# Performance work log

Measured on AMD Instinct MI355X. Metric: run time of the kernel, lower is better.

## Reference

```python
import jax, jax.numpy as jnp
import numpy as np

N = 100000   # num_nodes
E = 300000   # num directed edges (symmetrized to 2E inside forward)
D = 128      # input_dim
O = 128      # output_dim
R = 32       # num_relations
B = 8        # num_bases


def setup_inputs() -> dict:
    key = jax.random.key(0)
    ks = jax.random.split(key, 8)
    x = jax.random.normal(ks[0], (N, D), dtype=jnp.float32)
    node_keep_mask = jax.random.randint(ks[1], (N,), 0, 2) > 0
    source = jax.random.randint(ks[2], (E,), 0, N, dtype=jnp.int32)
    target = jax.random.randint(ks[3], (E,), 0, N, dtype=jnp.int32)
    edge_type = jax.random.randint(ks[4], (E,), 0, R, dtype=jnp.int32)
    edge_weights = jax.random.uniform(ks[5], (E,), dtype=jnp.float32)
    # xavier_normal for bases
    std = (2.0 / (D + O)) ** 0.5
    bases = jax.random.normal(ks[6], (B, D, O), dtype=jnp.float32) * std
    # uniform then L1-normalized rows, shape (R+1, B); row R is the self-loop
    rbw = jax.random.uniform(ks[7], (R + 1, B), dtype=jnp.float32)
    rbw = rbw / jnp.sum(rbw, axis=1, keepdims=True)
    return {
        "x": x,
        "node_keep_mask": node_keep_mask,
        "source": source,
        "target": target,
        "edge_type": edge_type,
        "edge_weights": edge_weights,
        "bases": bases,
        "relation_base_weights": rbw,
    }


def reference(x, node_keep_mask, source, target, edge_type, edge_weights,
              bases, relation_base_weights):
    # Self-loop: weight for relation id == num_relations (last row)
    w_self = jnp.einsum("bij,b->ij", bases, relation_base_weights[-1])
    out = jnp.where(node_keep_mask[:, None], x @ w_self, jnp.zeros((), x.dtype))

    # Symmetrize edges: messages flow in both directions (same relation/weight)
    src = jnp.concatenate([source, target])          # (2E,)
    tgt = jnp.concatenate([target, source])          # (2E,)
    etype = jnp.concatenate([edge_type, edge_type])  # (2E,)
    ew = jnp.concatenate([edge_weights, edge_weights])  # (2E,)

    # Project all nodes through every basis once: (N, B, O)
    proj = jnp.einsum("nd,bdo->nbo", x, bases)
    # Per-edge basis coefficients from the edge's relation: (2E, B)
    coeff = relation_base_weights[etype]
    # Message: x[src] @ (sum_b coeff_b * base_b) == sum_b coeff_b * proj[src, b]
    msg = jnp.einsum("eb,ebo->eo", coeff, proj[src])  # (2E, O)
    msg = msg * ew[:, None]

    # Scatter-add messages into target nodes
    out = out.at[tgt].add(msg)
    return out
```

## Files before the change

kernel.cpp:

```cpp
#include <hip/hip_runtime.h>

typedef __attribute__((ext_vector_type(8))) __bf16 bf16x8;
typedef __attribute__((ext_vector_type(4))) float f32x4;
typedef __attribute__((ext_vector_type(8))) unsigned short ushortx8;

#define MC 384
#define MCP 448

__device__ inline unsigned short f2bf(float f) {
  unsigned int u = __float_as_uint(f);
  unsigned int r = (u + 0x7FFFu + ((u >> 16) & 1u)) >> 16;
  return (unsigned short)r;
}
__device__ inline float bflo(unsigned u) { return __uint_as_float(u << 16); }
__device__ inline float bfhi(unsigned u) { return __uint_as_float(u & 0xFFFF0000u); }

__global__ __launch_bounds__(256) void prep_kernel(const float* __restrict__ x,
                                                   unsigned short* __restrict__ xb, int total8,
                                                   const float* __restrict__ bases,
                                                   unsigned short* __restrict__ bmt,
                                                   const int* __restrict__ src,
                                                   const int* __restrict__ tgt, int E,
                                                   int* __restrict__ cnt,
                                                   const unsigned char* __restrict__ mask,
                                                   int mbytes, int* __restrict__ flag_out,
                                                   int CB, int TB, int HB) {
  int bid = blockIdx.x;
  if (bid < CB) {
    int id = bid * 256 + threadIdx.x;
    if (id >= total8) return;
    f32x4 f0 = ((const f32x4*)x)[2 * id];
    f32x4 f1 = ((const f32x4*)x)[2 * id + 1];
    ushortx8 r;
    r[0] = f2bf(f0[0]); r[1] = f2bf(f0[1]); r[2] = f2bf(f0[2]); r[3] = f2bf(f0[3]);
    r[4] = f2bf(f1[0]); r[5] = f2bf(f1[1]); r[6] = f2bf(f1[2]); r[7] = f2bf(f1[3]);
    ((ushortx8*)xb)[id] = r;
  } else if (bid < CB + TB) {
    int id = (bid - CB) * 256 + threadIdx.x;
    if (id >= 128 * 1024) return;
    int o = id >> 10, k = id & 1023, b = k >> 7, d = k & 127;
    bmt[id] = f2bf(bases[b * 16384 + d * 128 + o]);
  } else if (bid < CB + TB + HB) {
    int i = (bid - CB - TB) * 256 + threadIdx.x;
    if (i >= E) return;
    atomicAdd(&cnt[tgt[i]], 1);
    atomicAdd(&cnt[src[i]], 1);
  } else {
    __shared__ int nz_off, big;
    if (threadIdx.x == 0) { nz_off = 0; big = 0; }
    __syncthreads();
    int lnz = 0, lbig = 0;
    for (int i = threadIdx.x; i < mbytes; i += 256) {
      unsigned char v = mask[i];
      if ((i & 3) && v) lnz++;
      if (v > 1) lbig++;
    }
    if (lnz) atomicAdd(&nz_off, lnz);
    if (lbig) atomicAdd(&big, lbig);
    __syncthreads();
    if (threadIdx.x == 0) *flag_out = (nz_off == 0) ? 0 : ((big == 0) ? 1 : 2);
  }
}

__global__ __launch_bounds__(256) void scanA_kernel(const int* __restrict__ cnt, int N,
                                                    int* __restrict__ bsum) {
  __shared__ int s[256];
  int t = threadIdx.x, i = blockIdx.x * 256 + t;
  s[t] = (i < N) ? cnt[i] : 0;
  __syncthreads();
#pragma unroll
  for (int off = 128; off > 0; off >>= 1) {
    if (t < off) s[t] += s[t + off];
    __syncthreads();
  }
  if (t == 0) bsum[blockIdx.x] = s[0];
}

__global__ __launch_bounds__(256) void scanB_kernel(const int* __restrict__ cnt, int N,
                                                    const int* __restrict__ bsum, int NB,
                                                    int* __restrict__ base,
                                                    int* __restrict__ cursor) {
  __shared__ int s[256];
  __shared__ int spref;
  int t = threadIdx.x, bid = blockIdx.x;
  int acc = 0;
  for (int i = t; i < bid; i += 256) acc += bsum[i];
  s[t] = acc;
  __syncthreads();
#pragma unroll
  for (int off = 128; off > 0; off >>= 1) {
    if (t < off) s[t] += s[t + off];
    __syncthreads();
  }
  if (t == 0) spref = s[0];
  __syncthreads();
  int pref = spref;
  __syncthreads();
  int i = bid * 256 + t;
  int c = (i < N) ? cnt[i] : 0;
  s[t] = c;
  __syncthreads();
  for (int off = 1; off < 256; off <<= 1) {
    int x = (t >= off) ? s[t - off] : 0;
    __syncthreads();
    s[t] += x;
    __syncthreads();
  }
  if (i < N) {
    int v = pref + s[t] - c;
    base[i] = v;
    cursor[i] = v;
  }
  if (bid == NB - 1 && t == 255) base[N] = pref + s[255];
}

__global__ __launch_bounds__(256) void scatter_kernel(const int* __restrict__ src,
                                                      const int* __restrict__ tgt,
                                                      const int* __restrict__ et,
                                                      const float* __restrict__ ew, int E,
                                                      const float* __restrict__ rbw,
                                                      int* __restrict__ cursor,
                                                      unsigned* __restrict__ msrc,
                                                      uint4* __restrict__ mcoef) {
  __shared__ float ctab[264];
  for (int i = threadIdx.x; i < 264; i += 256) ctab[i] = rbw[i];
  __syncthreads();
  if (blockIdx.x == 0 && threadIdx.x < 80) {
    msrc[2 * E + threadIdx.x] = 0u;
    mcoef[2 * E + threadIdx.x] = make_uint4(0u, 0u, 0u, 0u);
  }
  int i = blockIdx.x * 256 + threadIdx.x;
  if (i >= E) return;
  int s = src[i], g = tgt[i], r = et[i];
  float w = ew[i];
  uint4 cv;
  {
    const float* c = &ctab[r * 8];
    cv.x = (unsigned)f2bf(w * c[0]) | ((unsigned)f2bf(w * c[1]) << 16);
    cv.y = (unsigned)f2bf(w * c[2]) | ((unsigned)f2bf(w * c[3]) << 16);
    cv.z = (unsigned)f2bf(w * c[4]) | ((unsigned)f2bf(w * c[5]) << 16);
    cv.w = (unsigned)f2bf(w * c[6]) | ((unsigned)f2bf(w * c[7]) << 16);
  }
  int s1 = atomicAdd(&cursor[g], 1);
  msrc[s1] = (unsigned)s;
  mcoef[s1] = cv;
  int s2 = atomicAdd(&cursor[s], 1);
  msrc[s2] = (unsigned)g;
  mcoef[s2] = cv;
}

template <bool LDSM>
__device__ __forceinline__ void load4(const uint2* __restrict__ xb64,
                                      const unsigned* lms, const unsigned* __restrict__ gms,
                                      int B0, int gcap, int locS, int mb, int ll,
                                      unsigned Nm1, uint2 (&xq)[4]) {
#pragma unroll
  for (int s = 0; s < 4; ++s) {
    int idx = locS + mb + s;
    unsigned row;
    if (LDSM) row = lms[min(idx, MCP - 1)];
    else      row = gms[min(B0 + idx, gcap)];
    row = min(row & 0xFFFFFu, Nm1);
    xq[s] = xb64[(size_t)row * 32 + ll];
  }
}

template <bool LDSM>
__device__ __forceinline__ void fma4(const uint4* lmc, const uint4* __restrict__ gmc,
                                     int B0, int gcap, int locS, int cntS, int mb,
                                     const uint2 (&xq)[4], f32x4 (&z)[8]) {
#pragma unroll
  for (int s = 0; s < 4; ++s) {
    int idx = locS + mb + s;
    uint4 cf;
    if (LDSM) cf = lmc[min(idx, MCP - 1)];
    else      cf = gmc[min(B0 + idx, gcap)];
    unsigned vm = ((mb + s) < cntS) ? 0xFFFFFFFFu : 0u;
    unsigned c0 = cf.x & vm, c1 = cf.y & vm, c2 = cf.z & vm, c3 = cf.w & vm;
    f32x4 xv = {bflo(xq[s].x), bfhi(xq[s].x), bflo(xq[s].y), bfhi(xq[s].y)};
    float a;
    a = bflo(c0); z[0] = __builtin_elementwise_fma((f32x4){a, a, a, a}, xv, z[0]);
    a = bfhi(c0); z[1] = __builtin_elementwise_fma((f32x4){a, a, a, a}, xv, z[1]);
    a = bflo(c1); z[2] = __builtin_elementwise_fma((f32x4){a, a, a, a}, xv, z[2]);
    a = bfhi(c1); z[3] = __builtin_elementwise_fma((f32x4){a, a, a, a}, xv, z[3]);
    a = bflo(c2); z[4] = __builtin_elementwise_fma((f32x4){a, a, a, a}, xv, z[4]);
    a = bfhi(c2); z[5] = __builtin_elementwise_fma((f32x4){a, a, a, a}, xv, z[5]);
    a = bflo(c3); z[6] = __builtin_elementwise_fma((f32x4){a, a, a, a}, xv, z[6]);
    a = bfhi(c3); z[7] = __builtin_elementwise_fma((f32x4){a, a, a, a}, xv, z[7]);
  }
}

template <bool LDSM>
__device__ __forceinline__ void duo_loop(const uint2* __restrict__ xb64,
                                         const unsigned* lms, const uint4* lmc,
                                         const unsigned* __restrict__ gms,
                                         const uint4* __restrict__ gmc,
                                         int B0, int gcap, int locS, int cntS, int rmax,
                                         int ll, unsigned Nm1, f32x4 (&z)[8]) {
  int rounds = (rmax + 3) >> 2;
  if (rounds <= 0) return;
  uint2 xq0[4], xq1[4];
  load4<LDSM>(xb64, lms, gms, B0, gcap, locS, 0, ll, Nm1, xq0);
  for (int r = 0; r < rounds; ++r) {
    if ((r & 1) == 0) {
      if (r + 1 < rounds) load4<LDSM>(xb64, lms, gms, B0, gcap, locS, (r + 1) * 4, ll, Nm1, xq1);
      fma4<LDSM>(lmc, gmc, B0, gcap, locS, cntS, r * 4, xq0, z);
    } else {
      if (r + 1 < rounds) load4<LDSM>(xb64, lms, gms, B0, gcap, locS, (r + 1) * 4, ll, Nm1, xq0);
      fma4<LDSM>(lmc, gmc, B0, gcap, locS, cntS, r * 4, xq1, z);
    }
  }
}

__global__ __launch_bounds__(512, 4) void gather_kernel(
    const uint2* __restrict__ xb64, const unsigned short* __restrict__ bmt,
    const int* __restrict__ base, const unsigned* __restrict__ msrc,
    const uint4* __restrict__ mcoef, const float* __restrict__ rbw,
    const void* __restrict__ maskp, const int* __restrict__ flag_p,
    float* __restrict__ out, int N, int gcap) {
  extern __shared__ char smem[];
  unsigned* lms = (unsigned*)(smem + 65536);
  uint4* lmc = (uint4*)(smem + 65536 + MCP * 4);
  int* lbase = (int*)(smem + 65536 + MCP * 4 + MCP * 16);
  int t = threadIdx.x;
  int wid = t >> 6, l = t & 63;
  int hw = l >> 5, ll = l & 31;
  int t0 = blockIdx.x * 32;
  int flag = *flag_p;
  unsigned Nm1 = (unsigned)(N - 1);

  if (t < 33) lbase[t] = base[min(t0 + t, N)];
  int B0 = __builtin_amdgcn_readfirstlane(base[min(t0, N)]);
  int B1 = __builtin_amdgcn_readfirstlane(base[min(t0 + 32, N)]);
  int nm = B1 - B0;
  bool use_lds = (nm <= MC);
  if (use_lds) {
    for (int i = t; i < nm; i += 512) {
      lms[i] = msrc[B0 + i];
      lmc[i] = mcoef[B0 + i];
    }
    int pz = nm + t;
    if (t < 64 && pz < MCP) {
      lms[pz] = 0u;
      lmc[pz] = make_uint4(0u, 0u, 0u, 0u);
    }
  }
  __syncthreads();

  for (int p = 0; p < 2; ++p) {
    int jA = wid * 4 + p * 2, jB = jA + 1;
    int tgA = t0 + jA, tgB = t0 + jB;
    int begA = __builtin_amdgcn_readfirstlane(lbase[jA]);
    int begB = __builtin_amdgcn_readfirstlane(lbase[jB]);
    int endB = __builtin_amdgcn_readfirstlane(lbase[jB + 1]);
    int cntA = (tgA < N) ? (begB - begA) : 0;
    int cntB = (tgB < N) ? (endB - begB) : 0;
    int locA = begA - B0, locB = begB - B0;
    int tgS = hw ? tgB : tgA;
    int tcS = min(tgS, N - 1);
    int locS = hw ? locB : locA;
    int cntS = hw ? cntB : cntA;
    uint2 xs = xb64[(size_t)tcS * 32 + ll];
    int keep;
    if (flag == 0)      keep = ((const int*)maskp)[tcS] != 0;
    else if (flag == 1) keep = ((const unsigned char*)maskp)[tcS] != 0;
    else                keep = ((const float*)maskp)[tcS] != 0.f;
    float ms = (keep && tgS < N) ? 1.f : 0.f;
    f32x4 xv0 = {bflo(xs.x), bfhi(xs.x), bflo(xs.y), bfhi(xs.y)};
    f32x4 z[8];
#pragma unroll
    for (int b = 0; b < 8; ++b) {
      float a = ms * rbw[256 + b];
      z[b] = (f32x4){a, a, a, a} * xv0;
    }
    int rmax = max(cntA, cntB);
    if (use_lds)
      duo_loop<true>(xb64, lms, lmc, msrc, mcoef, B0, gcap, locS, cntS, rmax, ll, Nm1, z);
    else
      duo_loop<false>(xb64, lms, lmc, msrc, mcoef, B0, gcap, locS, cntS, rmax, ll, Nm1, z);
    int rowS = hw ? jB : jA;
#pragma unroll
    for (int b = 0; b < 8; ++b) {
      unsigned d0 = (unsigned)f2bf(z[b][0]) | ((unsigned)f2bf(z[b][1]) << 16);
      unsigned d1 = (unsigned)f2bf(z[b][2]) | ((unsigned)f2bf(z[b][3]) << 16);
      int byte = rowS * 2048 + ((b * 256 + ll * 8) ^ ((rowS & 7) << 4));
      *(uint2*)(smem + byte) = make_uint2(d0, d1);
    }
  }
  __syncthreads();

  int l15 = l & 15, lk8 = (l >> 4) * 8;
  f32x4 acc[2] = {};
  for (int ks = 0; ks < 32; ++ks) {
    int k0 = ks * 32 + lk8;
    bf16x8 a[2], bb;
#pragma unroll
    for (int rt = 0; rt < 2; ++rt) {
      int tr = rt * 16 + l15;
      int byte = tr * 2048 + ((k0 * 2) ^ ((tr & 7) << 4));
      a[rt] = *(const bf16x8*)(smem + byte);
    }
    int col = wid * 16 + l15;
    bb = *(const bf16x8*)(bmt + (size_t)col * 1024 + k0);
#pragma unroll
    for (int rt = 0; rt < 2; ++rt)
      acc[rt] = __builtin_amdgcn_mfma_f32_16x16x32_bf16(a[rt], bb, acc[rt], 0, 0, 0);
  }
#pragma unroll
  for (int rt = 0; rt < 2; ++rt) {
    int rowb = t0 + rt * 16 + (l >> 4) * 4;
    int col = wid * 16 + l15;
#pragma unroll
    for (int i = 0; i < 4; ++i) {
      int row = rowb + i;
      if (row < N) out[(size_t)row * 128 + col] = acc[rt][i];
    }
  }
}

extern "C" void kernel_launch(void* const* d_in, const int* in_sizes, int n_in,
                              void* d_out, int out_size, void* d_ws, size_t ws_size,
                              hipStream_t stream) {
  const float* x = (const float*)d_in[0];
  const void* mask = d_in[1];
  const int* source = (const int*)d_in[2];
  const int* target = (const int*)d_in[3];
  const int* etype = (const int*)d_in[4];
  const float* eweight = (const float*)d_in[5];
  const float* bases = (const float*)d_in[6];
  const float* rbw = (const float*)d_in[7];
  float* out = (float*)d_out;

  const int N = in_sizes[1];
  const int E = in_sizes[2];
  const int M = 2 * E;
  const int NB = (N + 255) / 256;

  char* ws = (char*)d_ws;
  size_t off = 0;
  unsigned short* xb = (unsigned short*)(ws + off); off += (size_t)N * 256;
  unsigned short* bmt = (unsigned short*)(ws + off); off += 128 * 1024 * 2;
  unsigned* msrc = (unsigned*)(ws + off); off += (size_t)(M + 96) * 4;
  uint4* mcoef = (uint4*)(ws + off); off += (size_t)(M + 96) * 16;
  int* base = (int*)(ws + off); off += ((size_t)N + 64) * 4;
  int* cursor = (int*)(ws + off); off += ((size_t)N + 64) * 4;
  int* cnt = (int*)(ws + off); off += ((size_t)N + 64) * 4;
  int* bsum = (int*)(ws + off); off += 2048;
  int* flag = (int*)(ws + off); off += 256;

  hipMemsetAsync(cnt, 0, (size_t)N * 4, stream);
  int total8 = (N * 128) / 8;
  int CB = (total8 + 255) / 256;
  int TB = (128 * 1024 + 255) / 256;
  int HB = (E + 255) / 256;
  prep_kernel<<<CB + TB + HB + 1, 256, 0, stream>>>(x, xb, total8, bases, bmt,
                                                    source, target, E, cnt,
                                                    (const unsigned char*)mask,
                                                    N < 8192 ? N : 8192, flag, CB, TB, HB);
  scanA_kernel<<<NB, 256, 0, stream>>>(cnt, N, bsum);
  scanB_kernel<<<NB, 256, 0, stream>>>(cnt, N, bsum, NB, base, cursor);
  scatter_kernel<<<(E + 255) / 256, 256, 0, stream>>>(source, target, etype, eweight, E,
                                                      rbw, cursor, msrc, mcoef);
  int gblk = (N + 31) / 32;
  size_t shmem = 65536 + MCP * 4 + MCP * 16 + 136;
  gather_kernel<<<gblk, 512, shmem, stream>>>((const uint2*)xb, bmt, base, msrc, mcoef,
                                              rbw, mask, flag, out, N, M + 79);
}
```

Before: 236.6 us.

## Fuse two node-pair gather passes into one triple-buffered prefetch pipeline

The gather phase used to run two separate passes per wave, each with its own double-buffered prefetch loop. It now runs a single continuous loop over the rounds of both node pairs, with a three-deep prefetch ring, and flushes and reseeds the accumulators at the boundary between pairs. This keeps row loads in flight across the pair boundary and hides more latency, at the cost of more registers and per-round select logic. Separately, the bases transpose in the prep kernel now goes through a 32x33 shared-memory tile so that both reads and writes are coalesced.

```diff
diff --git a/kernel.cpp b/kernel.cpp
--- a/kernel.cpp
+++ b/kernel.cpp
@@ -25,6 +25,8 @@
                                                    const unsigned char* __restrict__ mask,
                                                    int mbytes, int* __restrict__ flag_out,
                                                    int CB, int TB, int HB) {
+  __shared__ float tile_s[32][33];
+  __shared__ int nz_off, big;
   int bid = blockIdx.x;
   if (bid < CB) {
     int id = bid * 256 + threadIdx.x;
@@ -36,17 +38,27 @@
     r[4] = f2bf(f1[0]); r[5] = f2bf(f1[1]); r[6] = f2bf(f1[2]); r[7] = f2bf(f1[3]);
     ((ushortx8*)xb)[id] = r;
   } else if (bid < CB + TB) {
-    int id = (bid - CB) * 256 + threadIdx.x;
-    if (id >= 128 * 1024) return;
-    int o = id >> 10, k = id & 1023, b = k >> 7, d = k & 127;
-    bmt[id] = f2bf(bases[b * 16384 + d * 128 + o]);
+    int bid2 = bid - CB;
+    int b = bid2 >> 4, tile = bid2 & 15;
+    int o0 = (tile >> 2) * 32, d0 = (tile & 3) * 32;
+    int tx = threadIdx.x & 31, ty = threadIdx.x >> 5;
+#pragma unroll
+    for (int i = 0; i < 4; ++i) {
+      int dl = ty + i * 8;
+      tile_s[dl][tx] = bases[b * 16384 + (d0 + dl) * 128 + (o0 + tx)];
+    }
+    __syncthreads();
+#pragma unroll
+    for (int i = 0; i < 4; ++i) {
+      int ol = ty + i * 8;
+      bmt[(size_t)(o0 + ol) * 1024 + b * 128 + d0 + tx] = f2bf(tile_s[tx][ol]);
+    }
   } else if (bid < CB + TB + HB) {
     int i = (bid - CB - TB) * 256 + threadIdx.x;
     if (i >= E) return;
     atomicAdd(&cnt[tgt[i]], 1);
     atomicAdd(&cnt[src[i]], 1);
   } else {
-    __shared__ int nz_off, big;
     if (threadIdx.x == 0) { nz_off = 0; big = 0; }
     __syncthreads();
     int lnz = 0, lbig = 0;
@@ -150,13 +162,17 @@
 }
 
 template <bool LDSM>
-__device__ __forceinline__ void load4(const uint2* __restrict__ xb64,
-                                      const unsigned* lms, const unsigned* __restrict__ gms,
-                                      int B0, int gcap, int locS, int mb, int ll,
-                                      unsigned Nm1, uint2 (&xq)[4]) {
+__device__ __forceinline__ void pf_round(const uint2* __restrict__ xb64,
+                                         const unsigned* lms, const unsigned* __restrict__ gms,
+                                         int B0, int gcap, int R0, int RT,
+                                         int loc0, int loc1, int q, int ll, unsigned Nm1,
+                                         uint2 (&xq)[4]) {
+  int qq = min(q, RT - 1);
+  int loc = (qq < R0) ? loc0 : loc1;
+  int m = ((qq < R0) ? qq : qq - R0) * 4;
 #pragma unroll
   for (int s = 0; s < 4; ++s) {
-    int idx = locS + mb + s;
+    int idx = loc + m + s;
     unsigned row;
     if (LDSM) row = lms[min(idx, MCP - 1)];
     else      row = gms[min(B0 + idx, gcap)];
@@ -166,16 +182,20 @@
 }
 
 template <bool LDSM>
-__device__ __forceinline__ void fma4(const uint4* lmc, const uint4* __restrict__ gmc,
-                                     int B0, int gcap, int locS, int cntS, int mb,
-                                     const uint2 (&xq)[4], f32x4 (&z)[8]) {
+__device__ __forceinline__ void fma_round(const uint4* lmc, const uint4* __restrict__ gmc,
+                                          int B0, int gcap, int R0,
+                                          int loc0, int cnt0, int loc1, int cnt1,
+                                          int r, const uint2 (&xq)[4], f32x4 (&z)[8]) {
+  int loc = (r < R0) ? loc0 : loc1;
+  int cnt = (r < R0) ? cnt0 : cnt1;
+  int mb = ((r < R0) ? r : r - R0) * 4;
 #pragma unroll
   for (int s = 0; s < 4; ++s) {
-    int idx = locS + mb + s;
+    int idx = loc + mb + s;
     uint4 cf;
     if (LDSM) cf = lmc[min(idx, MCP - 1)];
     else      cf = gmc[min(B0 + idx, gcap)];
-    unsigned vm = ((mb + s) < cntS) ? 0xFFFFFFFFu : 0u;
+    unsigned vm = ((mb + s) < cnt) ? 0xFFFFFFFFu : 0u;
     unsigned c0 = cf.x & vm, c1 = cf.y & vm, c2 = cf.z & vm, c3 = cf.w & vm;
     f32x4 xv = {bflo(xq[s].x), bfhi(xq[s].x), bflo(xq[s].y), bfhi(xq[s].y)};
     float a;
@@ -190,26 +210,59 @@
   }
 }
 
+__device__ __forceinline__ void seed_z(const float* __restrict__ rbw, float ms, uint2 xs,
+                                       f32x4 (&z)[8]) {
+  f32x4 xv0 = {bflo(xs.x), bfhi(xs.x), bflo(xs.y), bfhi(xs.y)};
+#pragma unroll
+  for (int b = 0; b < 8; ++b) {
+    float a = ms * rbw[256 + b];
+    z[b] = (f32x4){a, a, a, a} * xv0;
+  }
+}
+
+__device__ __forceinline__ void flush_z(char* smem, int rowS, int ll, const f32x4 (&z)[8]) {
+#pragma unroll
+  for (int b = 0; b < 8; ++b) {
+    unsigned d0 = (unsigned)f2bf(z[b][0]) | ((unsigned)f2bf(z[b][1]) << 16);
+    unsigned d1 = (unsigned)f2bf(z[b][2]) | ((unsigned)f2bf(z[b][3]) << 16);
+    int byte = rowS * 2048 + ((b * 256 + ll * 8) ^ ((rowS & 7) << 4));
+    *(uint2*)(smem + byte) = make_uint2(d0, d1);
+  }
+}
+
 template <bool LDSM>
-__device__ __forceinline__ void duo_loop(const uint2* __restrict__ xb64,
-                                         const unsigned* lms, const uint4* lmc,
-                                         const unsigned* __restrict__ gms,
-                                         const uint4* __restrict__ gmc,
-                                         int B0, int gcap, int locS, int cntS, int rmax,
-                                         int ll, unsigned Nm1, f32x4 (&z)[8]) {
-  int rounds = (rmax + 3) >> 2;
-  if (rounds <= 0) return;
-  uint2 xq0[4], xq1[4];
-  load4<LDSM>(xb64, lms, gms, B0, gcap, locS, 0, ll, Nm1, xq0);
-  for (int r = 0; r < rounds; ++r) {
-    if ((r & 1) == 0) {
-      if (r + 1 < rounds) load4<LDSM>(xb64, lms, gms, B0, gcap, locS, (r + 1) * 4, ll, Nm1, xq1);
-      fma4<LDSM>(lmc, gmc, B0, gcap, locS, cntS, r * 4, xq0, z);
-    } else {
-      if (r + 1 < rounds) load4<LDSM>(xb64, lms, gms, B0, gcap, locS, (r + 1) * 4, ll, Nm1, xq0);
-      fma4<LDSM>(lmc, gmc, B0, gcap, locS, cntS, r * 4, xq1, z);
-    }
-  }
+__device__ __forceinline__ void wave_gather(const uint2* __restrict__ xb64,
+                                            const unsigned* lms, const uint4* lmc,
+                                            const unsigned* __restrict__ gms,
+                                            const uint4* __restrict__ gmc,
+                                            char* smem, const float* __restrict__ rbw,
+                                            int B0, int gcap, int R0, int RT,
+                                            int loc0, int cnt0, int loc1, int cnt1,
+                                            int row0, int row1, float ms0, float ms1,
+                                            uint2 xs0, uint2 xs1, int ll, unsigned Nm1) {
+  f32x4 z[8];
+  uint2 q0[4], q1[4], q2[4];
+#define PF(q_, buf_) pf_round<LDSM>(xb64, lms, gms, B0, gcap, R0, RT, loc0, loc1, (q_), ll, Nm1, buf_)
+#define FMAR(r_, buf_) fma_round<LDSM>(lmc, gmc, B0, gcap, R0, loc0, cnt0, loc1, cnt1, (r_), buf_, z)
+#define BNDRY(r_) if ((r_) == R0) { flush_z(smem, row0, ll, z); seed_z(rbw, ms1, xs1, z); }
+  if (RT > 0) { PF(0, q0); PF(1, q1); }
+  seed_z(rbw, ms0, xs0, z);
+  int r = 0;
+  while (r + 3 <= RT) {
+    PF(r + 2, q2); BNDRY(r); FMAR(r, q0);
+    PF(r + 3, q0); BNDRY(r + 1); FMAR(r + 1, q1);
+    PF(r + 4, q1); BNDRY(r + 2); FMAR(r + 2, q2);
+    r += 3;
+  }
+  if (r < RT) {
+    BNDRY(r); FMAR(r, q0); ++r;
+    if (r < RT) { BNDRY(r); FMAR(r, q1); ++r; }
+  }
+  if (R0 == RT) { flush_z(smem, row0, ll, z); seed_z(rbw, ms1, xs1, z); }
+  flush_z(smem, row1, ll, z);
+#undef PF
+#undef FMAR
+#undef BNDRY
 }
 
 __global__ __launch_bounds__(512, 4) void gather_kernel(
@@ -247,45 +300,45 @@
   }
   __syncthreads();
 
-  for (int p = 0; p < 2; ++p) {
-    int jA = wid * 4 + p * 2, jB = jA + 1;
-    int tgA = t0 + jA, tgB = t0 + jB;
-    int begA = __builtin_amdgcn_readfirstlane(lbase[jA]);
-    int begB = __builtin_amdgcn_readfirstlane(lbase[jB]);
-    int endB = __builtin_amdgcn_readfirstlane(lbase[jB + 1]);
-    int cntA = (tgA < N) ? (begB - begA) : 0;
-    int cntB = (tgB < N) ? (endB - begB) : 0;
-    int locA = begA - B0, locB = begB - B0;
-    int tgS = hw ? tgB : tgA;
-    int tcS = min(tgS, N - 1);
-    int locS = hw ? locB : locA;
-    int cntS = hw ? cntB : cntA;
-    uint2 xs = xb64[(size_t)tcS * 32 + ll];
-    int keep;
-    if (flag == 0)      keep = ((const int*)maskp)[tcS] != 0;
-    else if (flag == 1) keep = ((const unsigned char*)maskp)[tcS] != 0;
-    else                keep = ((const float*)maskp)[tcS] != 0.f;
-    float ms = (keep && tgS < N) ? 1.f : 0.f;
-    f32x4 xv0 = {bflo(xs.x), bfhi(xs.x), bflo(xs.y), bfhi(xs.y)};
-    f32x4 z[8];
-#pragma unroll
-    for (int b = 0; b < 8; ++b) {
-      float a = ms * rbw[256 + b];
-      z[b] = (f32x4){a, a, a, a} * xv0;
-    }
-    int rmax = max(cntA, cntB);
+  {
+    int jA0 = wid * 4;
+    int g0 = __builtin_amdgcn_readfirstlane(lbase[jA0]);
+    int g1 = __builtin_amdgcn_readfirstlane(lbase[jA0 + 1]);
+    int g2 = __builtin_amdgcn_readfirstlane(lbase[jA0 + 2]);
+    int g3 = __builtin_amdgcn_readfirstlane(lbase[jA0 + 3]);
+    int g4 = __builtin_amdgcn_readfirstlane(lbase[jA0 + 4]);
+    int tgb = t0 + jA0;
+    int cA0 = (tgb < N) ? (g1 - g0) : 0;
+    int cB0 = (tgb + 1 < N) ? (g2 - g1) : 0;
+    int cA1 = (tgb + 2 < N) ? (g3 - g2) : 0;
+    int cB1 = (tgb + 3 < N) ? (g4 - g3) : 0;
+    int lA0 = g0 - B0, lB0 = g1 - B0, lA1 = g2 - B0, lB1 = g3 - B0;
+    int loc0 = hw ? lB0 : lA0, cnt0 = hw ? cB0 : cA0;
+    int loc1 = hw ? lB1 : lA1, cnt1 = hw ? cB1 : cA1;
+    int row0 = jA0 + hw, row1 = jA0 + 2 + hw;
+    int tgS0 = t0 + row0, tgS1 = t0 + row1;
+    int tc0 = min(tgS0, N - 1), tc1 = min(tgS1, N - 1);
+    int R0 = (max(cA0, cB0) + 3) >> 2;
+    int R1 = (max(cA1, cB1) + 3) >> 2;
+    int RT = R0 + R1;
+    uint2 xs0 = xb64[(size_t)tc0 * 32 + ll];
+    uint2 xs1 = xb64[(size_t)tc1 * 32 + ll];
+    int k0, k1;
+    if (flag == 0) {
+      k0 = ((const int*)maskp)[tc0] != 0; k1 = ((const int*)maskp)[tc1] != 0;
+    } else if (flag == 1) {
+      k0 = ((const unsigned char*)maskp)[tc0] != 0; k1 = ((const unsigned char*)maskp)[tc1] != 0;
+    } else {
+      k0 = ((const float*)maskp)[tc0] != 0.f; k1 = ((const float*)maskp)[tc1] != 0.f;
+    }
+    float ms0 = (k0 && tgS0 < N) ? 1.f : 0.f;
+    float ms1 = (k1 && tgS1 < N) ? 1.f : 0.f;
     if (use_lds)
-      duo_loop<true>(xb64, lms, lmc, msrc, mcoef, B0, gcap, locS, cntS, rmax, ll, Nm1, z);
+      wave_gather<true>(xb64, lms, lmc, msrc, mcoef, smem, rbw, B0, gcap, R0, RT,
+                        loc0, cnt0, loc1, cnt1, row0, row1, ms0, ms1, xs0, xs1, ll, Nm1);
     else
-      duo_loop<false>(xb64, lms, lmc, msrc, mcoef, B0, gcap, locS, cntS, rmax, ll, Nm1, z);
-    int rowS = hw ? jB : jA;
-#pragma unroll
-    for (int b = 0; b < 8; ++b) {
-      unsigned d0 = (unsigned)f2bf(z[b][0]) | ((unsigned)f2bf(z[b][1]) << 16);
-      unsigned d1 = (unsigned)f2bf(z[b][2]) | ((unsigned)f2bf(z[b][3]) << 16);
-      int byte = rowS * 2048 + ((b * 256 + ll * 8) ^ ((rowS & 7) << 4));
-      *(uint2*)(smem + byte) = make_uint2(d0, d1);
-    }
+      wave_gather<false>(xb64, lms, lmc, msrc, mcoef, smem, rbw, B0, gcap, R0, RT,
+                         loc0, cnt0, loc1, cnt1, row0, row1, ms0, ms1, xs0, xs1, ll, Nm1);
   }
   __syncthreads();
 
@@ -351,7 +404,7 @@
   hipMemsetAsync(cnt, 0, (size_t)N * 4, stream);
   int total8 = (N * 128) / 8;
   int CB = (total8 + 255) / 256;
-  int TB = (128 * 1024 + 255) / 256;
+  int TB = 128;
   int HB = (E + 255) / 256;
   prep_kernel<<<CB + TB + HB + 1, 256, 0, stream>>>(x, xb, total8, bases, bmt,
                                                     source, target, E, cnt,
```

Measured after the change: 275.3 us. +16.3%, slower.
